# Performance work log

Measured on AMD Instinct MI355X. Metric: run time of the kernel, lower is better.

The kernel has to match this reference:

```python
import jax, jax.numpy as jnp
import numpy as np

N, E, B, H, L = 100000, 800000, 64, 128, 3
NC = 8  # num_classes
HT = H // 2  # trackster hidden
PD = 2 * H + HT  # pooled feature dim = 320


def layer_norm(h, g, b, eps=1e-5):
    mu = jnp.mean(h, axis=-1, keepdims=True)
    var = jnp.mean((h - mu) ** 2, axis=-1, keepdims=True)
    return (h - mu) / jnp.sqrt(var + eps) * g + b


def setup_inputs() -> dict:
    key = jax.random.key(0)
    ks = jax.random.split(key, 20)

    def xavier(k, shape):
        lim = np.sqrt(6.0 / (shape[-2] + shape[-1])).astype(np.float32)
        return jax.random.uniform(k, shape, jnp.float32, -lim, lim)

    return {
        "x": jax.random.normal(ks[0], (N, 4), jnp.float32),
        "edge_index": jax.random.randint(ks[1], (2, E), 0, N, jnp.int32),
        "batch": jnp.sort(jax.random.randint(ks[2], (N,), 0, B, jnp.int32)),
        "ts": jax.random.normal(ks[3], (B, 3), jnp.float32),
        # node encoder
        "enc_W": xavier(ks[4], (4, H)), "enc_b": jnp.zeros((H,), jnp.float32),
        # SAGEConv layers: lin_l (neighbors, with bias), lin_r (root, no bias)
        "sage_Wl": xavier(ks[5], (L, H, H)), "sage_bl": jnp.zeros((L, H), jnp.float32),
        "sage_Wr": xavier(ks[6], (L, H, H)),
        "ln_g": jnp.ones((L, H), jnp.float32), "ln_b": jnp.zeros((L, H), jnp.float32),
        # trackster encoder
        "ts_W1": xavier(ks[7], (3, HT)), "ts_b1": jnp.zeros((HT,), jnp.float32),
        "ts_lng": jnp.ones((HT,), jnp.float32), "ts_lnb": jnp.zeros((HT,), jnp.float32),
        "ts_W2": xavier(ks[8], (HT, HT)), "ts_b2": jnp.zeros((HT,), jnp.float32),
        # classifier
        "cls_lng": jnp.ones((PD,), jnp.float32), "cls_lnb": jnp.zeros((PD,), jnp.float32),
        "cls_W1": xavier(ks[9], (PD, H)), "cls_b1": jnp.zeros((H,), jnp.float32),
        "cls_W2": xavier(ks[10], (H, NC)), "cls_b2": jnp.zeros((NC,), jnp.float32),
    }


def reference(x, edge_index, batch, ts, enc_W, enc_b, sage_Wl, sage_bl, sage_Wr,
              ln_g, ln_b, ts_W1, ts_b1, ts_lng, ts_lnb, ts_W2, ts_b2,
              cls_lng, cls_lnb, cls_W1, cls_b1, cls_W2, cls_b2):
    src, dst = edge_index[0], edge_index[1]
    h = jax.nn.relu(x @ enc_W + enc_b)  # [N, H]
    # in-degree for mean aggregation (isolated nodes -> aggr 0, like PyG)
    deg = jnp.maximum(jax.ops.segment_sum(jnp.ones((E,), h.dtype), dst, num_segments=N), 1.0)
    for i in range(L):
        agg = jax.ops.segment_sum(h[src], dst, num_segments=N) / deg[:, None]  # mean over in-neighbors
        hn = agg @ sage_Wl[i] + sage_bl[i] + h @ sage_Wr[i]  # SAGEConv
        hn = layer_norm(hn, ln_g[i], ln_b[i])
        h = h + jax.nn.relu(hn)  # dropout is identity in eval
    # dense-pool == segment mean + segment max per graph
    cnt = jnp.maximum(jax.ops.segment_sum(jnp.ones((N,), h.dtype), batch, num_segments=B), 1.0)
    g_mean = jax.ops.segment_sum(h, batch, num_segments=B) / cnt[:, None]  # [B, H]
    g_max = jax.ops.segment_max(h, batch, num_segments=B)  # [B, H]
    # trackster encoder
    t = ts @ ts_W1 + ts_b1
    t = jax.nn.relu(layer_norm(t, ts_lng, ts_lnb))
    t = t @ ts_W2 + ts_b2  # [B, HT]
    feat = jnp.concatenate([g_mean, g_max, t], axis=1)  # [B, 320]
    z = layer_norm(feat, cls_lng, cls_lnb)
    z = jax.nn.relu(z @ cls_W1 + cls_b1)
    return z @ cls_W2 + cls_b2  # [B, NC]
```

## Files before the change

### kernel.cpp

```cpp
#include <hip/hip_runtime.h>
#include <hip/hip_bf16.h>

#define HH 128
#define BUK_SH 9
#define BUK 512
#define CAP 8192

typedef __attribute__((ext_vector_type(8))) short short8;
typedef __attribute__((ext_vector_type(4))) float floatx4;

__device__ __forceinline__ ushort f2bf(float f) {
    uint u = __float_as_uint(f);
    uint r = (u + 0x7FFFu + ((u >> 16) & 1u)) >> 16;
    return (ushort)r;
}
__device__ __forceinline__ float bflo(uint p) { return __uint_as_float(p << 16); }
__device__ __forceinline__ float bfhi(uint p) { return __uint_as_float(p & 0xFFFF0000u); }
__device__ __forceinline__ uint packbf(float a, float b) {
    return (uint)f2bf(a) | ((uint)f2bf(b) << 16);
}


__global__ __launch_bounds__(256) void bin_k(
    const int* __restrict__ src, const int* __restrict__ dst,
    int* __restrict__ gcur, uint* __restrict__ ebuf, int E) {
    __shared__ int hist[256];
    __shared__ int base[256];
    int tid = threadIdx.x;
    hist[tid] = 0;
    __syncthreads();
    int e0 = blockIdx.x * 2048;
    int d[8];
#pragma unroll
    for (int i = 0; i < 8; i++) {
        int e = e0 + i * 256 + tid;
        d[i] = (e < E) ? dst[e] : -1;
        if (d[i] >= 0) atomicAdd(&hist[d[i] >> BUK_SH], 1);
    }
    __syncthreads();
    if (hist[tid] > 0) base[tid] = atomicAdd(&gcur[tid], hist[tid]);
    hist[tid] = 0;
    __syncthreads();
#pragma unroll
    for (int i = 0; i < 8; i++) {
        if (d[i] >= 0) {
            int e = e0 + i * 256 + tid;
            int b = d[i] >> BUK_SH;
            int p = base[b] + atomicAdd(&hist[b], 1);
            if (p < CAP)
                ebuf[(size_t)b * CAP + p] = ((uint)(d[i] & (BUK - 1)) << 17) | (uint)src[e];
        }
    }
}

__global__ void bscan_k(const int* __restrict__ gcur, int* __restrict__ bbase, int nbuk) {
    __shared__ int s[256];
    int t = threadIdx.x;
    int v = (t < nbuk) ? gcur[t] : 0;
    s[t] = v;
    __syncthreads();
    for (int o = 1; o < 256; o <<= 1) {
        int tv = (t >= o) ? s[t - o] : 0;
        __syncthreads();
        s[t] += tv;
        __syncthreads();
    }
    if (t < nbuk) bbase[t] = s[t] - v;
}

__global__ __launch_bounds__(256) void build_k(
    const uint* __restrict__ ebuf, const int* __restrict__ gcur,
    const int* __restrict__ bbase, int* __restrict__ offs, float* __restrict__ invd,
    int* __restrict__ csr, int N, int nbuk) {
    __shared__ int ncnt[BUK];
    __shared__ int npre[BUK];
    __shared__ int ss[256];
    __shared__ int csrbuf[CAP];
    int b = blockIdx.x, tid = threadIdx.x;
    int cnt = gcur[b]; if (cnt > CAP) cnt = CAP;
    int base = bbase[b];
    ncnt[tid] = 0; ncnt[tid + 256] = 0;
    __syncthreads();
    const uint* eb = ebuf + (size_t)b * CAP;
    for (int i = tid; i < cnt; i += 256) atomicAdd(&ncnt[eb[i] >> 17], 1);
    __syncthreads();
    int a0 = ncnt[2 * tid], a1 = ncnt[2 * tid + 1];
    int pair = a0 + a1;
    ss[tid] = pair;
    __syncthreads();
    for (int o = 1; o < 256; o <<= 1) {
        int tv = (tid >= o) ? ss[tid - o] : 0;
        __syncthreads();
        ss[tid] += tv;
        __syncthreads();
    }
    int ep = ss[tid] - pair;
    npre[2 * tid] = ep;
    npre[2 * tid + 1] = ep + a0;
    __syncthreads();
#pragma unroll
    for (int q = 0; q < 2; q++) {
        int ln = q * 256 + tid;
        int node = b * BUK + ln;
        if (node < N) {
            offs[node] = base + npre[ln];
            int dg = ncnt[ln];
            invd[node] = 1.0f / (float)(dg > 1 ? dg : 1);
        }
    }
    __syncthreads();
    ncnt[2 * tid] = npre[2 * tid];
    ncnt[2 * tid + 1] = npre[2 * tid + 1];
    __syncthreads();
    for (int i = tid; i < cnt; i += 256) {
        uint pk = eb[i];
        int p = atomicAdd(&ncnt[pk >> 17], 1);
        csrbuf[p] = (int)(pk & 0x1FFFFu);
    }
    __syncthreads();
    for (int i = tid; i < cnt; i += 256) csr[base + i] = csrbuf[i];
    if (b == nbuk - 1 && tid == 0) offs[N] = base + cnt;
}


__global__ __launch_bounds__(256) void prep_w_k(
    const float* __restrict__ Wl, const float* __restrict__ Wr, ushort* __restrict__ Bp) {
    int gid = blockIdx.x * 256 + threadIdx.x;
    int layer = gid >> 15;
    int r = gid & 32767;
    int j = r & 7;
    int lane = (r >> 3) & 63;
    int ct = (r >> 9) & 7;
    int ks = r >> 12;
    int k = ks * 32 + (lane >> 4) * 8 + j;
    int n = ct * 16 + (lane & 15);
    float v = (k < HH) ? Wl[(size_t)layer * HH * HH + k * HH + n]
                       : Wr[(size_t)layer * HH * HH + (k - HH) * HH + n];
    Bp[gid] = f2bf(v);
}


__global__ __launch_bounds__(256) void encoder_k(
    const float* __restrict__ x, const float* __restrict__ W,
    const float* __restrict__ b, float* __restrict__ h, uint* __restrict__ hb, int N) {
    int n = blockIdx.x * 4 + (threadIdx.x >> 6);
    int j = threadIdx.x & 63;
    if (n >= N) return;
    float4 xv = *(const float4*)(x + (size_t)n * 4);
    float v0 = b[2 * j], v1 = b[2 * j + 1];
    v0 = fmaf(xv.x, W[0 * HH + 2 * j], v0); v1 = fmaf(xv.x, W[0 * HH + 2 * j + 1], v1);
    v0 = fmaf(xv.y, W[1 * HH + 2 * j], v0); v1 = fmaf(xv.y, W[1 * HH + 2 * j + 1], v1);
    v0 = fmaf(xv.z, W[2 * HH + 2 * j], v0); v1 = fmaf(xv.z, W[2 * HH + 2 * j + 1], v1);
    v0 = fmaf(xv.w, W[3 * HH + 2 * j], v0); v1 = fmaf(xv.w, W[3 * HH + 2 * j + 1], v1);
    v0 = fmaxf(v0, 0.0f); v1 = fmaxf(v1, 0.0f);
    h[(size_t)n * HH + 2 * j] = v0;
    h[(size_t)n * HH + 2 * j + 1] = v1;
    hb[(size_t)n * 64 + j] = packbf(v0, v1);
}


__global__ __launch_bounds__(256) void aggregate_k(
    const uint* __restrict__ hb, const int* __restrict__ offs,
    const int* __restrict__ csr, const float* __restrict__ invd,
    uint* __restrict__ aggb, int N) {
    int n = blockIdx.x * 16 + (threadIdx.x >> 4);
    int j = threadIdx.x & 15;
    if (n >= N) return;
    const uint4* hb4 = (const uint4*)hb;
    int s = offs[n], e = offs[n + 1];
    float a0 = 0, a1 = 0, a2 = 0, a3 = 0, a4 = 0, a5 = 0, a6 = 0, a7 = 0;
    int i = s;
    for (; i + 4 <= e; i += 4) {
        int u0 = csr[i], u1 = csr[i + 1], u2 = csr[i + 2], u3 = csr[i + 3];
        uint4 p0 = hb4[(size_t)u0 * 16 + j];
        uint4 p1 = hb4[(size_t)u1 * 16 + j];
        uint4 p2 = hb4[(size_t)u2 * 16 + j];
        uint4 p3 = hb4[(size_t)u3 * 16 + j];
        a0 += (bflo(p0.x) + bflo(p1.x)) + (bflo(p2.x) + bflo(p3.x));
        a1 += (bfhi(p0.x) + bfhi(p1.x)) + (bfhi(p2.x) + bfhi(p3.x));
        a2 += (bflo(p0.y) + bflo(p1.y)) + (bflo(p2.y) + bflo(p3.y));
        a3 += (bfhi(p0.y) + bfhi(p1.y)) + (bfhi(p2.y) + bfhi(p3.y));
        a4 += (bflo(p0.z) + bflo(p1.z)) + (bflo(p2.z) + bflo(p3.z));
        a5 += (bfhi(p0.z) + bfhi(p1.z)) + (bfhi(p2.z) + bfhi(p3.z));
        a6 += (bflo(p0.w) + bflo(p1.w)) + (bflo(p2.w) + bflo(p3.w));
        a7 += (bfhi(p0.w) + bfhi(p1.w)) + (bfhi(p2.w) + bfhi(p3.w));
    }
    for (; i < e; i++) {
        uint4 p = hb4[(size_t)csr[i] * 16 + j];
        a0 += bflo(p.x); a1 += bfhi(p.x);
        a2 += bflo(p.y); a3 += bfhi(p.y);
        a4 += bflo(p.z); a5 += bfhi(p.z);
        a6 += bflo(p.w); a7 += bfhi(p.w);
    }
    float iv = invd[n];
    uint4 o;
    o.x = packbf(a0 * iv, a1 * iv);
    o.y = packbf(a2 * iv, a3 * iv);
    o.z = packbf(a4 * iv, a5 * iv);
    o.w = packbf(a6 * iv, a7 * iv);
    ((uint4*)aggb)[(size_t)n * 16 + j] = o;
}


__global__ __launch_bounds__(256) void sage_mfma_k(
    const ushort* __restrict__ aggb, float* __restrict__ h, ushort* __restrict__ hb,
    const ushort* __restrict__ Bp, const float* __restrict__ bl,
    const float* __restrict__ g, const float* __restrict__ bln, int N) {
    int wave = threadIdx.x >> 6;
    int lane = threadIdx.x & 63;
    int m0 = blockIdx.x * 128 + wave * 32;

    floatx4 acc[2][8];
#pragma unroll
    for (int rt = 0; rt < 2; rt++)
#pragma unroll
        for (int ct = 0; ct < 8; ct++) acc[rt][ct] = (floatx4)0.0f;

    int am = lane & 15, aq = lane >> 4;
#pragma unroll
    for (int ks = 0; ks < 8; ks++) {
        const ushort* Asrc = (ks < 4) ? aggb : (const ushort*)hb;
        int kc = (ks & 3) * 32 + aq * 8;
        short8 a[2];
#pragma unroll
        for (int rt = 0; rt < 2; rt++) {
            int row = m0 + rt * 16 + am;
            row = row < N ? row : N - 1;
            a[rt] = *(const short8*)(Asrc + (size_t)row * HH + kc);
        }
#pragma unroll
        for (int ct = 0; ct < 8; ct++) {
            short8 b = *(const short8*)(Bp + (((size_t)(ks * 8 + ct)) * 64 + lane) * 8);
            acc[0][ct] = __builtin_amdgcn_mfma_f32_16x16x32_bf16(a[0], b, acc[0][ct], 0, 0, 0);
            acc[1][ct] = __builtin_amdgcn_mfma_f32_16x16x32_bf16(a[1], b, acc[1][ct], 0, 0, 0);
        }
    }

    int g4 = lane >> 4, cl = lane & 15;
    float bias[8], gam[8], bet[8];
#pragma unroll
    for (int ct = 0; ct < 8; ct++) {
        bias[ct] = bl[ct * 16 + cl];
        gam[ct] = g[ct * 16 + cl];
        bet[ct] = bln[ct * 16 + cl];
    }
#pragma unroll
    for (int rt = 0; rt < 2; rt++) {
        float sr[4], qr[4];
#pragma unroll
        for (int reg = 0; reg < 4; reg++) {
            float s = 0.0f, q = 0.0f;
#pragma unroll
            for (int ct = 0; ct < 8; ct++) {
                float v = acc[rt][ct][reg] + bias[ct];
                s += v;
                q += v * v;
            }
#pragma unroll
            for (int m = 1; m < 16; m <<= 1) {
                s += __shfl_xor(s, m);
                q += __shfl_xor(q, m);
            }
            sr[reg] = s;
            qr[reg] = q;
        }
#pragma unroll
        for (int reg = 0; reg < 4; reg++) {
            int row = m0 + rt * 16 + g4 * 4 + reg;
            if (row < N) {
                float mean = sr[reg] * (1.0f / 128.0f);
                float var = qr[reg] * (1.0f / 128.0f) - mean * mean;
                float rstd = rsqrtf(fmaxf(var, 0.0f) + 1e-5f);
#pragma unroll
                for (int ct = 0; ct < 8; ct++) {
                    float v = acc[rt][ct][reg] + bias[ct];
                    float r = fmaxf((v - mean) * rstd * gam[ct] + bet[ct], 0.0f);
                    size_t idx = (size_t)row * HH + ct * 16 + cl;
                    float nv = h[idx] + r;
                    h[idx] = nv;
                    hb[idx] = f2bf(nv);
                }
            }
        }
    }
}


__global__ __launch_bounds__(256) void pool_k(
    const uint* __restrict__ hb, const int* __restrict__ batch,
    float* __restrict__ psum, int* __restrict__ pmax, int* __restrict__ pcnt, int N) {
    __shared__ float ls[8][32][4];
    __shared__ float lm[8][32][4];
    int tid = threadIdx.x;
    int lane = tid & 31;
    int slot = tid >> 5;
    int n0 = blockIdx.x * 256;
    int nlast = n0 + 255 < N - 1 ? n0 + 255 : N - 1;
    const uint2* hb2 = (const uint2*)hb;
    int b0 = batch[n0];

    if (batch[nlast] == b0) {
        float s0 = 0, s1 = 0, s2 = 0, s3 = 0, m0 = 0, m1 = 0, m2 = 0, m3 = 0;
        for (int i = 0; i < 32; i++) {
            int n = n0 + i * 8 + slot;
            if (n < N) {
                uint2 p = hb2[(size_t)n * 32 + lane];
                float v0 = bflo(p.x), v1 = bfhi(p.x), v2 = bflo(p.y), v3 = bfhi(p.y);
                s0 += v0; s1 += v1; s2 += v2; s3 += v3;
                m0 = fmaxf(m0, v0); m1 = fmaxf(m1, v1);
                m2 = fmaxf(m2, v2); m3 = fmaxf(m3, v3);
            }
        }
        ls[slot][lane][0] = s0; ls[slot][lane][1] = s1;
        ls[slot][lane][2] = s2; ls[slot][lane][3] = s3;
        lm[slot][lane][0] = m0; lm[slot][lane][1] = m1;
        lm[slot][lane][2] = m2; lm[slot][lane][3] = m3;
        __syncthreads();
        if (tid < 128) {
            int ln = tid >> 2, c = tid & 3;
            float s = 0.0f, m = 0.0f;
#pragma unroll
            for (int sl = 0; sl < 8; sl++) {
                s += ls[sl][ln][c];
                m = fmaxf(m, lm[sl][ln][c]);
            }
            atomicAdd(&psum[b0 * HH + tid], s);
            atomicMax(&pmax[b0 * HH + tid], __float_as_int(m));
        }
        if (tid == 0) {
            int rows = (N - n0 < 256) ? (N - n0) : 256;
            atomicAdd(&pcnt[b0], rows);
        }
    } else {
        int cur = -1, run = 0;
        float s0 = 0, s1 = 0, s2 = 0, s3 = 0, m0 = 0, m1 = 0, m2 = 0, m3 = 0;
        for (int i = 0; i < 32; i++) {
            int n = n0 + i * 8 + slot;
            if (n >= N) break;
            int b = batch[n];
            if (b != cur) {
                if (cur >= 0) {
                    int cb = cur * HH + lane * 4;
                    atomicAdd(&psum[cb + 0], s0);
                    atomicAdd(&psum[cb + 1], s1);
                    atomicAdd(&psum[cb + 2], s2);
                    atomicAdd(&psum[cb + 3], s3);
                    atomicMax(&pmax[cb + 0], __float_as_int(m0));
                    atomicMax(&pmax[cb + 1], __float_as_int(m1));
                    atomicMax(&pmax[cb + 2], __float_as_int(m2));
                    atomicMax(&pmax[cb + 3], __float_as_int(m3));
                    if (lane == 0) atomicAdd(&pcnt[cur], run);
                }
                cur = b;
                s0 = s1 = s2 = s3 = 0.0f;
                m0 = m1 = m2 = m3 = 0.0f;
                run = 0;
            }
            uint2 p = hb2[(size_t)n * 32 + lane];
            float v0 = bflo(p.x), v1 = bfhi(p.x), v2 = bflo(p.y), v3 = bfhi(p.y);
            s0 += v0; s1 += v1; s2 += v2; s3 += v3;
            m0 = fmaxf(m0, v0); m1 = fmaxf(m1, v1);
            m2 = fmaxf(m2, v2); m3 = fmaxf(m3, v3);
            run++;
        }
        if (cur >= 0) {
            int cb = cur * HH + lane * 4;
            atomicAdd(&psum[cb + 0], s0);
            atomicAdd(&psum[cb + 1], s1);
            atomicAdd(&psum[cb + 2], s2);
            atomicAdd(&psum[cb + 3], s3);
            atomicMax(&pmax[cb + 0], __float_as_int(m0));
            atomicMax(&pmax[cb + 1], __float_as_int(m1));
            atomicMax(&pmax[cb + 2], __float_as_int(m2));
            atomicMax(&pmax[cb + 3], __float_as_int(m3));
            if (lane == 0) atomicAdd(&pcnt[cur], run);
        }
    }
}


__global__ __launch_bounds__(128) void head_k(
    const float* __restrict__ psum, const float* __restrict__ pmax,
    const int* __restrict__ pcnt, const float* __restrict__ ts,
    const float* __restrict__ tsW1, const float* __restrict__ tsb1,
    const float* __restrict__ tslng, const float* __restrict__ tslnb,
    const float* __restrict__ tsW2, const float* __restrict__ tsb2,
    const float* __restrict__ clng, const float* __restrict__ clnb,
    const float* __restrict__ cW1, const float* __restrict__ cb1,
    const float* __restrict__ cW2, const float* __restrict__ cb2,
    float* __restrict__ out) {
    int b = blockIdx.x;
    int t = threadIdx.x;
    __shared__ float feat[320];
    __shared__ float tn[64];
    __shared__ float zz[128];
    __shared__ float ps[2], pq[2];

    if (t < 64) {
        float v = tsb1[t];
#pragma unroll
        for (int k = 0; k < 3; k++) v = fmaf(ts[b * 3 + k], tsW1[k * 64 + t], v);
        float s = v, q = v * v;
#pragma unroll
        for (int m = 1; m < 64; m <<= 1) {
            s += __shfl_xor(s, m);
            q += __shfl_xor(q, m);
        }
        float mean = s * (1.0f / 64.0f);
        float var = q * (1.0f / 64.0f) - mean * mean;
        float rstd = rsqrtf(fmaxf(var, 0.0f) + 1e-5f);
        tn[t] = fmaxf((v - mean) * rstd * tslng[t] + tslnb[t], 0.0f);
    }
    __syncthreads();
    if (t < 64) {
        float v = tsb2[t];
        for (int k = 0; k < 64; k++) v = fmaf(tn[k], tsW2[k * 64 + t], v);
        feat[256 + t] = v;
    }
    float cntf = (float)(pcnt[b] > 1 ? pcnt[b] : 1);
    feat[t] = psum[b * HH + t] / cntf;
    feat[128 + t] = pmax[b * HH + t];
    __syncthreads();

    float s = 0.0f, q = 0.0f;
    for (int i = t; i < 320; i += 128) {
        float v = feat[i];
        s += v;
        q += v * v;
    }
#pragma unroll
    for (int m = 1; m < 64; m <<= 1) {
        s += __shfl_xor(s, m);
        q += __shfl_xor(q, m);
    }
    if ((t & 63) == 0) { ps[t >> 6] = s; pq[t >> 6] = q; }
    __syncthreads();
    float S = ps[0] + ps[1], Q = pq[0] + pq[1];
    float mean = S * (1.0f / 320.0f);
    float var = Q * (1.0f / 320.0f) - mean * mean;
    float rstd = rsqrtf(fmaxf(var, 0.0f) + 1e-5f);
    for (int i = t; i < 320; i += 128)
        feat[i] = (feat[i] - mean) * rstd * clng[i] + clnb[i];
    __syncthreads();

    {
        float v = cb1[t];
        for (int k = 0; k < 320; k++) v = fmaf(feat[k], cW1[k * HH + t], v);
        zz[t] = fmaxf(v, 0.0f);
    }
    __syncthreads();
    if (t < 8) {
        float v = cb2[t];
        for (int k = 0; k < 128; k++) v = fmaf(zz[k], cW2[k * 8 + t], v);
        out[b * 8 + t] = v;
    }
}


extern "C" void kernel_launch(void* const* d_in, const int* in_sizes, int n_in,
                              void* d_out, int out_size, void* d_ws, size_t ws_size,
                              hipStream_t stream) {
    const int N = in_sizes[0] / 4;
    const int E = in_sizes[1] / 2;
    const int B = in_sizes[3] / 3;
    const int nbuk = (N + BUK - 1) >> BUK_SH;

    const float* x    = (const float*)d_in[0];
    const int*   ei   = (const int*)d_in[1];
    const int*   srcv = ei;
    const int*   dstv = ei + E;
    const int*   batch = (const int*)d_in[2];
    const float* ts   = (const float*)d_in[3];
    const float* encW = (const float*)d_in[4];
    const float* encb = (const float*)d_in[5];
    const float* sageWl = (const float*)d_in[6];
    const float* sagebl = (const float*)d_in[7];
    const float* sageWr = (const float*)d_in[8];
    const float* lng  = (const float*)d_in[9];
    const float* lnb  = (const float*)d_in[10];
    const float* tsW1 = (const float*)d_in[11];
    const float* tsb1 = (const float*)d_in[12];
    const float* tslng = (const float*)d_in[13];
    const float* tslnb = (const float*)d_in[14];
    const float* tsW2 = (const float*)d_in[15];
    const float* tsb2 = (const float*)d_in[16];
    const float* clng = (const float*)d_in[17];
    const float* clnb = (const float*)d_in[18];
    const float* cW1  = (const float*)d_in[19];
    const float* cb1  = (const float*)d_in[20];
    const float* cW2  = (const float*)d_in[21];
    const float* cb2  = (const float*)d_in[22];
    float* out = (float*)d_out;

    char* w = (char*)d_ws;
    size_t off = 0;
    auto take = [&](size_t bytes) -> void* {
        void* p = w + off;
        off = (off + bytes + 255) & ~(size_t)255;
        return p;
    };
    float* h    = (float*)take((size_t)N * HH * 4);
    uint*  hb   = (uint*)take((size_t)N * HH * 2);
    uint*  aggb = (uint*)take((size_t)N * HH * 2);
    ushort* Bp  = (ushort*)take((size_t)3 * HH * 2 * HH * 2);
    int*   csr  = (int*)take((size_t)E * 4);
    int*   offs = (int*)take((size_t)(N + 1) * 4);
    float* invd = (float*)take((size_t)N * 4);
    uint*  ebuf = (uint*)take((size_t)nbuk * CAP * 4);
    int*   gcur = (int*)take(256 * 4);
    int*   bbase = (int*)take(256 * 4);
    float* psum = (float*)take((size_t)B * HH * 4);
    int*   pmax = (int*)take((size_t)B * HH * 4);
    int*   pcnt = (int*)take((size_t)B * 4);

    hipMemsetAsync(gcur, 0, 256 * 4, stream);
    hipMemsetAsync(psum, 0, (size_t)B * HH * 4, stream);
    hipMemsetAsync(pmax, 0, (size_t)B * HH * 4, stream);
    hipMemsetAsync(pcnt, 0, (size_t)B * 4, stream);

    bin_k<<<(E + 2047) / 2048, 256, 0, stream>>>(srcv, dstv, gcur, ebuf, E);
    bscan_k<<<1, 256, 0, stream>>>(gcur, bbase, nbuk);
    build_k<<<nbuk, 256, 0, stream>>>(ebuf, gcur, bbase, offs, invd, csr, N, nbuk);

    prep_w_k<<<384, 256, 0, stream>>>(sageWl, sageWr, Bp);
    encoder_k<<<(N + 3) / 4, 256, 0, stream>>>(x, encW, encb, h, hb, N);

    for (int l = 0; l < 3; l++) {
        aggregate_k<<<(N + 15) / 16, 256, 0, stream>>>(hb, offs, csr, invd, aggb, N);
        sage_mfma_k<<<(N + 127) / 128, 256, 0, stream>>>(
            (const ushort*)aggb, h, (ushort*)hb, Bp + (size_t)l * 32768,
            sagebl + (size_t)l * HH, lng + (size_t)l * HH, lnb + (size_t)l * HH, N);
    }

    pool_k<<<(N + 255) / 256, 256, 0, stream>>>(hb, batch, psum, pmax, pcnt, N);
    head_k<<<B, 128, 0, stream>>>(psum, (const float*)pmax, pcnt, ts,
                                  tsW1, tsb1, tslng, tslnb, tsW2, tsb2,
                                  clng, clnb, cW1, cb1, cW2, cb2, out);
}
```

Before: 423.0 us.

## Fuse final SAGE layer with graph pooling, fold bucket scan into CSR build

```diff
diff --git a/kernel.cpp b/kernel.cpp
--- a/kernel.cpp
+++ b/kernel.cpp
@@ -53,32 +53,30 @@
     }
 }
 
-__global__ void bscan_k(const int* __restrict__ gcur, int* __restrict__ bbase, int nbuk) {
-    __shared__ int s[256];
-    int t = threadIdx.x;
-    int v = (t < nbuk) ? gcur[t] : 0;
-    s[t] = v;
-    __syncthreads();
-    for (int o = 1; o < 256; o <<= 1) {
-        int tv = (t >= o) ? s[t - o] : 0;
-        __syncthreads();
-        s[t] += tv;
-        __syncthreads();
-    }
-    if (t < nbuk) bbase[t] = s[t] - v;
-}
-
 __global__ __launch_bounds__(256) void build_k(
     const uint* __restrict__ ebuf, const int* __restrict__ gcur,
-    const int* __restrict__ bbase, int* __restrict__ offs, float* __restrict__ invd,
+    int* __restrict__ offs, float* __restrict__ invd,
     int* __restrict__ csr, int N, int nbuk) {
     __shared__ int ncnt[BUK];
     __shared__ int npre[BUK];
     __shared__ int ss[256];
     __shared__ int csrbuf[CAP];
     int b = blockIdx.x, tid = threadIdx.x;
+
+    int bc = (tid < nbuk) ? gcur[tid] : 0;
+    if (bc > CAP) bc = CAP;
+    ss[tid] = bc;
+    __syncthreads();
+    for (int o = 1; o < 256; o <<= 1) {
+        int tv = (tid >= o) ? ss[tid - o] : 0;
+        __syncthreads();
+        ss[tid] += tv;
+        __syncthreads();
+    }
     int cnt = gcur[b]; if (cnt > CAP) cnt = CAP;
-    int base = bbase[b];
+    int base = ss[b] - cnt;
+    __syncthreads();
+
     ncnt[tid] = 0; ncnt[tid + 256] = 0;
     __syncthreads();
     const uint* eb = ebuf + (size_t)b * CAP;
@@ -170,20 +168,35 @@
     int s = offs[n], e = offs[n + 1];
     float a0 = 0, a1 = 0, a2 = 0, a3 = 0, a4 = 0, a5 = 0, a6 = 0, a7 = 0;
     int i = s;
+    for (; i + 8 <= e; i += 8) {
+        int u[8];
+        uint4 p[8];
+#pragma unroll
+        for (int q = 0; q < 8; q++) u[q] = csr[i + q];
+#pragma unroll
+        for (int q = 0; q < 8; q++) p[q] = hb4[(size_t)u[q] * 16 + j];
+#pragma unroll
+        for (int q = 0; q < 8; q++) {
+            a0 += bflo(p[q].x); a1 += bfhi(p[q].x);
+            a2 += bflo(p[q].y); a3 += bfhi(p[q].y);
+            a4 += bflo(p[q].z); a5 += bfhi(p[q].z);
+            a6 += bflo(p[q].w); a7 += bfhi(p[q].w);
+        }
+    }
     for (; i + 4 <= e; i += 4) {
-        int u0 = csr[i], u1 = csr[i + 1], u2 = csr[i + 2], u3 = csr[i + 3];
-        uint4 p0 = hb4[(size_t)u0 * 16 + j];
-        uint4 p1 = hb4[(size_t)u1 * 16 + j];
-        uint4 p2 = hb4[(size_t)u2 * 16 + j];
-        uint4 p3 = hb4[(size_t)u3 * 16 + j];
-        a0 += (bflo(p0.x) + bflo(p1.x)) + (bflo(p2.x) + bflo(p3.x));
-        a1 += (bfhi(p0.x) + bfhi(p1.x)) + (bfhi(p2.x) + bfhi(p3.x));
-        a2 += (bflo(p0.y) + bflo(p1.y)) + (bflo(p2.y) + bflo(p3.y));
-        a3 += (bfhi(p0.y) + bfhi(p1.y)) + (bfhi(p2.y) + bfhi(p3.y));
-        a4 += (bflo(p0.z) + bflo(p1.z)) + (bflo(p2.z) + bflo(p3.z));
-        a5 += (bfhi(p0.z) + bfhi(p1.z)) + (bfhi(p2.z) + bfhi(p3.z));
-        a6 += (bflo(p0.w) + bflo(p1.w)) + (bflo(p2.w) + bflo(p3.w));
-        a7 += (bfhi(p0.w) + bfhi(p1.w)) + (bfhi(p2.w) + bfhi(p3.w));
+        int u[4];
+        uint4 p[4];
+#pragma unroll
+        for (int q = 0; q < 4; q++) u[q] = csr[i + q];
+#pragma unroll
+        for (int q = 0; q < 4; q++) p[q] = hb4[(size_t)u[q] * 16 + j];
+#pragma unroll
+        for (int q = 0; q < 4; q++) {
+            a0 += bflo(p[q].x); a1 += bfhi(p[q].x);
+            a2 += bflo(p[q].y); a3 += bfhi(p[q].y);
+            a4 += bflo(p[q].z); a5 += bfhi(p[q].z);
+            a6 += bflo(p[q].w); a7 += bfhi(p[q].w);
+        }
     }
     for (; i < e; i++) {
         uint4 p = hb4[(size_t)csr[i] * 16 + j];
@@ -286,95 +299,143 @@
 }
 
 
-__global__ __launch_bounds__(256) void pool_k(
-    const uint* __restrict__ hb, const int* __restrict__ batch,
+__global__ __launch_bounds__(256) void sage_pool_k(
+    const ushort* __restrict__ aggb, const float* __restrict__ h,
+    const ushort* __restrict__ hb, const ushort* __restrict__ Bp,
+    const float* __restrict__ bl, const float* __restrict__ g,
+    const float* __restrict__ bln, const int* __restrict__ batch,
     float* __restrict__ psum, int* __restrict__ pmax, int* __restrict__ pcnt, int N) {
-    __shared__ float ls[8][32][4];
-    __shared__ float lm[8][32][4];
+    __shared__ float tile[64][128];
+    __shared__ int bb[128];
     int tid = threadIdx.x;
-    int lane = tid & 31;
-    int slot = tid >> 5;
-    int n0 = blockIdx.x * 256;
-    int nlast = n0 + 255 < N - 1 ? n0 + 255 : N - 1;
-    const uint2* hb2 = (const uint2*)hb;
-    int b0 = batch[n0];
-
-    if (batch[nlast] == b0) {
-        float s0 = 0, s1 = 0, s2 = 0, s3 = 0, m0 = 0, m1 = 0, m2 = 0, m3 = 0;
-        for (int i = 0; i < 32; i++) {
-            int n = n0 + i * 8 + slot;
-            if (n < N) {
-                uint2 p = hb2[(size_t)n * 32 + lane];
-                float v0 = bflo(p.x), v1 = bfhi(p.x), v2 = bflo(p.y), v3 = bfhi(p.y);
-                s0 += v0; s1 += v1; s2 += v2; s3 += v3;
-                m0 = fmaxf(m0, v0); m1 = fmaxf(m1, v1);
-                m2 = fmaxf(m2, v2); m3 = fmaxf(m3, v3);
+    int wave = tid >> 6;
+    int lane = tid & 63;
+    int blk0 = blockIdx.x * 128;
+    int m0 = blk0 + wave * 32;
+
+    if (tid < 128) {
+        int r = blk0 + tid;
+        bb[tid] = (r < N) ? batch[r] : -1;
+    }
+
+    floatx4 acc[2][8];
+#pragma unroll
+    for (int rt = 0; rt < 2; rt++)
+#pragma unroll
+        for (int ct = 0; ct < 8; ct++) acc[rt][ct] = (floatx4)0.0f;
+
+    int am = lane & 15, aq = lane >> 4;
+#pragma unroll
+    for (int ks = 0; ks < 8; ks++) {
+        const ushort* Asrc = (ks < 4) ? aggb : hb;
+        int kc = (ks & 3) * 32 + aq * 8;
+        short8 a[2];
+#pragma unroll
+        for (int rt = 0; rt < 2; rt++) {
+            int row = m0 + rt * 16 + am;
+            row = row < N ? row : N - 1;
+            a[rt] = *(const short8*)(Asrc + (size_t)row * HH + kc);
+        }
+#pragma unroll
+        for (int ct = 0; ct < 8; ct++) {
+            short8 b = *(const short8*)(Bp + (((size_t)(ks * 8 + ct)) * 64 + lane) * 8);
+            acc[0][ct] = __builtin_amdgcn_mfma_f32_16x16x32_bf16(a[0], b, acc[0][ct], 0, 0, 0);
+            acc[1][ct] = __builtin_amdgcn_mfma_f32_16x16x32_bf16(a[1], b, acc[1][ct], 0, 0, 0);
+        }
+    }
+
+    int g4 = lane >> 4, cl = lane & 15;
+    float bias[8], gam[8], bet[8];
+#pragma unroll
+    for (int ct = 0; ct < 8; ct++) {
+        bias[ct] = bl[ct * 16 + cl];
+        gam[ct] = g[ct * 16 + cl];
+        bet[ct] = bln[ct * 16 + cl];
+    }
+#pragma unroll
+    for (int rt = 0; rt < 2; rt++) {
+        float sr[4], qr[4];
+#pragma unroll
+        for (int reg = 0; reg < 4; reg++) {
+            float s = 0.0f, q = 0.0f;
+#pragma unroll
+            for (int ct = 0; ct < 8; ct++) {
+                float v = acc[rt][ct][reg] + bias[ct];
+                s += v;
+                q += v * v;
             }
-        }
-        ls[slot][lane][0] = s0; ls[slot][lane][1] = s1;
-        ls[slot][lane][2] = s2; ls[slot][lane][3] = s3;
-        lm[slot][lane][0] = m0; lm[slot][lane][1] = m1;
-        lm[slot][lane][2] = m2; lm[slot][lane][3] = m3;
+#pragma unroll
+            for (int m = 1; m < 16; m <<= 1) {
+                s += __shfl_xor(s, m);
+                q += __shfl_xor(q, m);
+            }
+            sr[reg] = s;
+            qr[reg] = q;
+        }
+#pragma unroll
+        for (int reg = 0; reg < 4; reg++) {
+            int row = m0 + rt * 16 + g4 * 4 + reg;
+            float mean = sr[reg] * (1.0f / 128.0f);
+            float var = qr[reg] * (1.0f / 128.0f) - mean * mean;
+            float rstd = rsqrtf(fmaxf(var, 0.0f) + 1e-5f);
+            if (row < N) {
+#pragma unroll
+                for (int ct = 0; ct < 8; ct++) {
+                    float v = acc[rt][ct][reg] + bias[ct];
+                    float r = fmaxf((v - mean) * rstd * gam[ct] + bet[ct], 0.0f);
+                    acc[rt][ct][reg] = h[(size_t)row * HH + ct * 16 + cl] + r;
+                }
+            }
+        }
+    }
+    __syncthreads();
+
+    int cur = -1, run = 0;
+    float ps = 0.0f, pm = 0.0f;
+
+#pragma unroll
+    for (int phase = 0; phase < 2; phase++) {
+        if ((wave >> 1) == phase) {
+            int rbase = (wave & 1) * 32;
+#pragma unroll
+            for (int rt = 0; rt < 2; rt++)
+#pragma unroll
+                for (int reg = 0; reg < 4; reg++) {
+                    int rloc = rbase + rt * 16 + g4 * 4 + reg;
+                    if (blk0 + phase * 64 + rloc < N) {
+#pragma unroll
+                        for (int ct = 0; ct < 8; ct++)
+                            tile[rloc][ct * 16 + cl] = acc[rt][ct][reg];
+                    }
+                }
+        }
         __syncthreads();
         if (tid < 128) {
-            int ln = tid >> 2, c = tid & 3;
-            float s = 0.0f, m = 0.0f;
-#pragma unroll
-            for (int sl = 0; sl < 8; sl++) {
-                s += ls[sl][ln][c];
-                m = fmaxf(m, lm[sl][ln][c]);
+            int c = tid;
+            for (int r = 0; r < 64; r++) {
+                int b = bb[phase * 64 + r];
+                if (b < 0) break;
+                float v = tile[r][c];
+                if (b != cur) {
+                    if (cur >= 0) {
+                        atomicAdd(&psum[cur * HH + c], ps);
+                        atomicMax(&pmax[cur * HH + c], __float_as_int(pm));
+                        if (c == 0) atomicAdd(&pcnt[cur], run);
+                    }
+                    cur = b; ps = 0.0f; pm = 0.0f; run = 0;
+                }
+                ps += v;
+                pm = fmaxf(pm, v);
+                run++;
             }
-            atomicAdd(&psum[b0 * HH + tid], s);
-            atomicMax(&pmax[b0 * HH + tid], __float_as_int(m));
-        }
-        if (tid == 0) {
-            int rows = (N - n0 < 256) ? (N - n0) : 256;
-            atomicAdd(&pcnt[b0], rows);
-        }
-    } else {
-        int cur = -1, run = 0;
-        float s0 = 0, s1 = 0, s2 = 0, s3 = 0, m0 = 0, m1 = 0, m2 = 0, m3 = 0;
-        for (int i = 0; i < 32; i++) {
-            int n = n0 + i * 8 + slot;
-            if (n >= N) break;
-            int b = batch[n];
-            if (b != cur) {
-                if (cur >= 0) {
-                    int cb = cur * HH + lane * 4;
-                    atomicAdd(&psum[cb + 0], s0);
-                    atomicAdd(&psum[cb + 1], s1);
-                    atomicAdd(&psum[cb + 2], s2);
-                    atomicAdd(&psum[cb + 3], s3);
-                    atomicMax(&pmax[cb + 0], __float_as_int(m0));
-                    atomicMax(&pmax[cb + 1], __float_as_int(m1));
-                    atomicMax(&pmax[cb + 2], __float_as_int(m2));
-                    atomicMax(&pmax[cb + 3], __float_as_int(m3));
-                    if (lane == 0) atomicAdd(&pcnt[cur], run);
-                }
-                cur = b;
-                s0 = s1 = s2 = s3 = 0.0f;
-                m0 = m1 = m2 = m3 = 0.0f;
-                run = 0;
-            }
-            uint2 p = hb2[(size_t)n * 32 + lane];
-            float v0 = bflo(p.x), v1 = bfhi(p.x), v2 = bflo(p.y), v3 = bfhi(p.y);
-            s0 += v0; s1 += v1; s2 += v2; s3 += v3;
-            m0 = fmaxf(m0, v0); m1 = fmaxf(m1, v1);
-            m2 = fmaxf(m2, v2); m3 = fmaxf(m3, v3);
-            run++;
-        }
-        if (cur >= 0) {
-            int cb = cur * HH + lane * 4;
-            atomicAdd(&psum[cb + 0], s0);
-            atomicAdd(&psum[cb + 1], s1);
-            atomicAdd(&psum[cb + 2], s2);
-            atomicAdd(&psum[cb + 3], s3);
-            atomicMax(&pmax[cb + 0], __float_as_int(m0));
-            atomicMax(&pmax[cb + 1], __float_as_int(m1));
-            atomicMax(&pmax[cb + 2], __float_as_int(m2));
-            atomicMax(&pmax[cb + 3], __float_as_int(m3));
-            if (lane == 0) atomicAdd(&pcnt[cur], run);
-        }
+        }
+        __syncthreads();
+    }
+    if (tid < 128 && cur >= 0) {
+        int c = tid;
+        atomicAdd(&psum[cur * HH + c], ps);
+        atomicMax(&pmax[cur * HH + c], __float_as_int(pm));
+        if (c == 0) atomicAdd(&pcnt[cur], run);
     }
 }
 
@@ -507,32 +568,33 @@
     int*   offs = (int*)take((size_t)(N + 1) * 4);
     float* invd = (float*)take((size_t)N * 4);
     uint*  ebuf = (uint*)take((size_t)nbuk * CAP * 4);
+    size_t z0 = off;
     int*   gcur = (int*)take(256 * 4);
-    int*   bbase = (int*)take(256 * 4);
     float* psum = (float*)take((size_t)B * HH * 4);
     int*   pmax = (int*)take((size_t)B * HH * 4);
     int*   pcnt = (int*)take((size_t)B * 4);
-
-    hipMemsetAsync(gcur, 0, 256 * 4, stream);
-    hipMemsetAsync(psum, 0, (size_t)B * HH * 4, stream);
-    hipMemsetAsync(pmax, 0, (size_t)B * HH * 4, stream);
-    hipMemsetAsync(pcnt, 0, (size_t)B * 4, stream);
+    size_t z1 = off;
+
+    hipMemsetAsync(w + z0, 0, z1 - z0, stream);
 
     bin_k<<<(E + 2047) / 2048, 256, 0, stream>>>(srcv, dstv, gcur, ebuf, E);
-    bscan_k<<<1, 256, 0, stream>>>(gcur, bbase, nbuk);
-    build_k<<<nbuk, 256, 0, stream>>>(ebuf, gcur, bbase, offs, invd, csr, N, nbuk);
+    build_k<<<nbuk, 256, 0, stream>>>(ebuf, gcur, offs, invd, csr, N, nbuk);
 
     prep_w_k<<<384, 256, 0, stream>>>(sageWl, sageWr, Bp);
     encoder_k<<<(N + 3) / 4, 256, 0, stream>>>(x, encW, encb, h, hb, N);
 
-    for (int l = 0; l < 3; l++) {
+    for (int l = 0; l < 2; l++) {
         aggregate_k<<<(N + 15) / 16, 256, 0, stream>>>(hb, offs, csr, invd, aggb, N);
         sage_mfma_k<<<(N + 127) / 128, 256, 0, stream>>>(
             (const ushort*)aggb, h, (ushort*)hb, Bp + (size_t)l * 32768,
             sagebl + (size_t)l * HH, lng + (size_t)l * HH, lnb + (size_t)l * HH, N);
     }
-
-    pool_k<<<(N + 255) / 256, 256, 0, stream>>>(hb, batch, psum, pmax, pcnt, N);
+    aggregate_k<<<(N + 15) / 16, 256, 0, stream>>>(hb, offs, csr, invd, aggb, N);
+    sage_pool_k<<<(N + 127) / 128, 256, 0, stream>>>(
+        (const ushort*)aggb, h, (const ushort*)hb, Bp + (size_t)2 * 32768,
+        sagebl + (size_t)2 * HH, lng + (size_t)2 * HH, lnb + (size_t)2 * HH,
+        batch, psum, pmax, pcnt, N);
+
     head_k<<<B, 128, 0, stream>>>(psum, (const float*)pmax, pcnt, ts,
                                   tsW1, tsb1, tslng, tslnb, tsW2, tsb2,
                                   clng, clnb, cW1, cb1, cW2, cb2, out);
```

Measured after the change: 429.1 us. No clear change (+1.4%).
